# Performance work log

Hardware: AMD Instinct MI355X
Metric: run time of the kernel (lower is better)

## Reference

```python
import jax, jax.numpy as jnp
import numpy as np

B, N, D = 32, 256, 3
NF, L = 16, 3


def _fully_connected(n):
    # Same ordering as connect_fully: for i in range(n) for j in range(n) if i != j
    a = np.repeat(np.arange(n), n)
    b = np.tile(np.arange(n), n)
    m = a != b
    return a[m].astype(np.int32), b[m].astype(np.int32)


def setup_inputs() -> dict:
    key = jax.random.key(0)
    ks = jax.random.split(key, 12)
    src, dst = _fully_connected(N)
    s = 0.1  # small param scale for numerical stability
    return {
        "xs": jax.random.normal(ks[0], (B, N, D), jnp.float32),
        "vs": jax.random.normal(ks[1], (B, N, D), jnp.float32),
        "charges": jax.random.normal(ks[2], (B * N, 1), jnp.float32),
        "W_in": s * jax.random.normal(ks[3], (1, NF), jnp.float32),
        "b_in": jnp.zeros((NF,), jnp.float32),
        "W_v": s * jax.random.normal(ks[4], (L, NF, 1), jnp.float32),
        "We1": s * jax.random.normal(ks[5], (L, 2 * NF + 1, NF), jnp.float32),
        "be1": jnp.zeros((L, NF), jnp.float32),
        "We2": s * jax.random.normal(ks[6], (L, NF, NF), jnp.float32),
        "be2": jnp.zeros((L, NF), jnp.float32),
        "Wx": s * jax.random.normal(ks[7], (L, NF, 1), jnp.float32),
        "Wh1": s * jax.random.normal(ks[8], (L, 2 * NF, NF), jnp.float32),
        "bh1": jnp.zeros((L, NF), jnp.float32),
        "src": jnp.asarray(src),
        "dst": jnp.asarray(dst),
    }


def reference(xs, vs, charges, W_in, b_in, W_v, We1, be1, We2, be2, Wx, Wh1, bh1, src, dst):
    b, n, d = xs.shape
    # node scalar features from charges (ndata['f'])
    h = jax.nn.relu(charges.reshape(b, n, 1) @ W_in + b_in)  # [B,N,nf]
    x = xs
    n_layers = We1.shape[0]
    for l in range(n_layers):
        # fully-connected edge gather + subtract (edata['d'])
        de = x[:, dst] - x[:, src]                         # [B,E,3]
        r2 = jnp.sum(de * de, axis=-1, keepdims=True)      # [B,E,1]
        e_in = jnp.concatenate([h[:, src], h[:, dst], r2], axis=-1)  # [B,E,2nf+1]
        m = jax.nn.relu(e_in @ We1[l] + be1[l])
        m = jax.nn.relu(m @ We2[l] + be2[l])               # [B,E,nf]
        w = m @ Wx[l]                                      # [B,E,1]
        # equivariant coordinate update: scatter-add edge vectors into dst nodes
        agg_x = jnp.zeros_like(x).at[:, dst].add(de * w) / (n - 1)
        x = x + agg_x + vs * (h @ W_v[l])                  # velocity term (ndata['vel'])
        m_agg = jnp.zeros_like(h).at[:, dst].add(m)        # [B,N,nf]
        h = h + jax.nn.relu(jnp.concatenate([h, m_agg], axis=-1) @ Wh1[l] + bh1[l])
    # OurDynamics returns (se3_out['1'] + xs).view(-1, n_dimension)
    return x.reshape(-1, d)
```

## Files before the change

### kernel.cpp

```cpp
#include <hip/hip_runtime.h>

#define BB 32
#define NN 256
#define NF 16

typedef _Float16 half4 __attribute__((ext_vector_type(4)));
typedef float f32x4 __attribute__((ext_vector_type(4)));

#define X0_OFF 0
#define X1_OFF 32768
#define H0_OFF 65536
#define H1_OFF 196608
#define SU0_OFF 327680
#define SV0_OFF 458752
#define SU1_OFF 589824
#define SV1_OFF 720896
#define SU2_OFF 851968
#define SV2_OFF 983040

__global__ __launch_bounds__(256)
void init_kernel(const float* __restrict__ xs, const float* __restrict__ charges,
                 const float* __restrict__ W_in, const float* __restrict__ b_in,
                 const float* __restrict__ We1, const float* __restrict__ be1,
                 float* __restrict__ x0, float* __restrict__ h0,
                 float* __restrict__ su0, float* __restrict__ sv0) {
    __shared__ float sWs[256], sWd[256], sb1[NF];
    const int tid = threadIdx.x;
    sWs[tid] = We1[tid];
    sWd[tid] = We1[256 + tid];
    if (tid < NF) sb1[tid] = be1[tid];
    const int n = blockIdx.x * 256 + tid;
    const float c = charges[n];
    float h[NF];
#pragma unroll
    for (int f = 0; f < NF; ++f) {
        h[f] = fmaxf(fmaf(c, W_in[f], b_in[f]), 0.f);
        h0[n * NF + f] = h[f];
    }
    x0[n * 4 + 0] = xs[n * 3 + 0];
    x0[n * 4 + 1] = xs[n * 3 + 1];
    x0[n * 4 + 2] = xs[n * 3 + 2];
    x0[n * 4 + 3] = 0.f;
    __syncthreads();
#pragma unroll
    for (int k = 0; k < NF; ++k) {
        float u = 0.f, v = sb1[k];
#pragma unroll
        for (int f = 0; f < NF; ++f) {
            u = fmaf(h[f], sWs[f * NF + k], u);
            v = fmaf(h[f], sWd[f * NF + k], v);
        }
        su0[n * NF + k] = u;
        sv0[n * NF + k] = v;
    }
}

__global__ __launch_bounds__(256)
void layer_kernel(const float* __restrict__ x_in, const float* __restrict__ h_in,
                  const float* __restrict__ su_in, const float* __restrict__ sv_in,
                  float* __restrict__ x_out, float* __restrict__ h_out,
                  float* __restrict__ su_out, float* __restrict__ sv_out,
                  const float* __restrict__ vs, const float* __restrict__ Wv_l,
                  const float* __restrict__ We1_l, const float* __restrict__ We2_l,
                  const float* __restrict__ be2_l, const float* __restrict__ Wx_l,
                  const float* __restrict__ Wh1_l, const float* __restrict__ bh1_l,
                  const float* __restrict__ We1_n, const float* __restrict__ be1_n,
                  int final_layer) {
    __shared__ float sWh1s[512];
    __shared__ float sWa[256];
    __shared__ float sWb[256];
    __shared__ float sbe1n[NF];
    __shared__ float sh_new[8][NF + 1];
    __shared__ float sg[8][NF];

    const int tid  = threadIdx.x;
    const int b    = blockIdx.x >> 5;
    const int oct  = blockIdx.x & 31;
    const int n0l  = 8 * oct;
    const size_t n0 = (size_t)b * NN + n0l;
    const int w    = tid >> 6;
    const int lane = tid & 63;
    const int c    = lane & 15;
    const int g    = lane >> 4;

    sWh1s[tid]       = Wh1_l[tid];
    sWh1s[256 + tid] = Wh1_l[256 + tid];
    if (!final_layer) {
        const int f = tid >> 4, k = tid & 15;
        sWa[k * NF + f] = We1_n[tid];
        sWb[k * NF + f] = We1_n[256 + tid];
        if (tid < NF) sbe1n[tid] = be1_n[tid];
    }

    const int j0 = n0l + w, j1 = n0l + 4 + w;
    const float* x_b  = x_in + (size_t)b * NN * 4;
    const float* su_b = su_in + (size_t)b * NN * NF;
    const float4 xj0 = *(const float4*)(x_b + 4 * j0);
    const float4 xj1 = *(const float4*)(x_b + 4 * j1);
    half4 afrag;
    afrag.x = (_Float16)We2_l[(4 * g + 0) * NF + c];
    afrag.y = (_Float16)We2_l[(4 * g + 1) * NF + c];
    afrag.z = (_Float16)We2_l[(4 * g + 2) * NF + c];
    afrag.w = (_Float16)We2_l[(4 * g + 3) * NF + c];
    const float4 v40  = *(const float4*)(sv_in + ((size_t)b * NN + j0) * NF + 4 * g);
    const float4 v41  = *(const float4*)(sv_in + ((size_t)b * NN + j1) * NF + 4 * g);
    const float4 wr4  = *(const float4*)(We1_l + 512 + 4 * g);
    const float4 be2f = *(const float4*)(be2_l + 4 * g);
    const float4 wxf  = *(const float4*)(Wx_l + 4 * g);

    float Sw0 = 0.f, Swx0 = 0.f, Swy0 = 0.f, Swz0 = 0.f;
    float Sw1 = 0.f, Swx1 = 0.f, Swy1 = 0.f, Swz1 = 0.f;
    float g00 = 0.f, g01 = 0.f, g02 = 0.f, g03 = 0.f;
    float g10 = 0.f, g11 = 0.f, g12 = 0.f, g13 = 0.f;

    const float* su_p = su_b + c * NF + 4 * g;
    const float* x_p  = x_b + 4 * c;

#pragma unroll 2
    for (int t = 0; t < 16; ++t) {
        const float4 u4  = *(const float4*)(su_p + 256 * t);
        const float4 xs4 = *(const float4*)(x_p + 64 * t);
        const f32x4 zc = {0.f, 0.f, 0.f, 0.f};
        const int s = 16 * t + c;
        {
            const float dx = xj0.x - xs4.x, dy = xj0.y - xs4.y, dz = xj0.z - xs4.z;
            const float r2 = fmaf(dx, dx, fmaf(dy, dy, dz * dz));
            const float m0 = fmaxf(fmaf(r2, wr4.x, u4.x + v40.x), 0.f);
            const float m1 = fmaxf(fmaf(r2, wr4.y, u4.y + v40.y), 0.f);
            const float m2 = fmaxf(fmaf(r2, wr4.z, u4.z + v40.z), 0.f);
            const float m3 = fmaxf(fmaf(r2, wr4.w, u4.w + v40.w), 0.f);
            half4 bfrag;
            bfrag.x = (_Float16)m0; bfrag.y = (_Float16)m1;
            bfrag.z = (_Float16)m2; bfrag.w = (_Float16)m3;
            const f32x4 acc = __builtin_amdgcn_mfma_f32_16x16x16f16(afrag, bfrag, zc, 0, 0, 0);
            const float e0 = fmaxf(acc.x + be2f.x, 0.f);
            const float e1 = fmaxf(acc.y + be2f.y, 0.f);
            const float e2 = fmaxf(acc.z + be2f.z, 0.f);
            const float e3 = fmaxf(acc.w + be2f.w, 0.f);
            float wp = e0 * wxf.x;
            wp = fmaf(e1, wxf.y, wp);
            wp = fmaf(e2, wxf.z, wp);
            wp = fmaf(e3, wxf.w, wp);
            const float gsel = (s != j0) ? 1.f : 0.f;
            g00 = fmaf(e0, gsel, g00);
            g01 = fmaf(e1, gsel, g01);
            g02 = fmaf(e2, gsel, g02);
            g03 = fmaf(e3, gsel, g03);
            Sw0 += wp;
            Swx0 = fmaf(wp, xs4.x, Swx0);
            Swy0 = fmaf(wp, xs4.y, Swy0);
            Swz0 = fmaf(wp, xs4.z, Swz0);
        }
        {
            const float dx = xj1.x - xs4.x, dy = xj1.y - xs4.y, dz = xj1.z - xs4.z;
            const float r2 = fmaf(dx, dx, fmaf(dy, dy, dz * dz));
            const float m0 = fmaxf(fmaf(r2, wr4.x, u4.x + v41.x), 0.f);
            const float m1 = fmaxf(fmaf(r2, wr4.y, u4.y + v41.y), 0.f);
            const float m2 = fmaxf(fmaf(r2, wr4.z, u4.z + v41.z), 0.f);
            const float m3 = fmaxf(fmaf(r2, wr4.w, u4.w + v41.w), 0.f);
            half4 bfrag;
            bfrag.x = (_Float16)m0; bfrag.y = (_Float16)m1;
            bfrag.z = (_Float16)m2; bfrag.w = (_Float16)m3;
            const f32x4 acc = __builtin_amdgcn_mfma_f32_16x16x16f16(afrag, bfrag, zc, 0, 0, 0);
            const float e0 = fmaxf(acc.x + be2f.x, 0.f);
            const float e1 = fmaxf(acc.y + be2f.y, 0.f);
            const float e2 = fmaxf(acc.z + be2f.z, 0.f);
            const float e3 = fmaxf(acc.w + be2f.w, 0.f);
            float wp = e0 * wxf.x;
            wp = fmaf(e1, wxf.y, wp);
            wp = fmaf(e2, wxf.z, wp);
            wp = fmaf(e3, wxf.w, wp);
            const float gsel = (s != j1) ? 1.f : 0.f;
            g10 = fmaf(e0, gsel, g10);
            g11 = fmaf(e1, gsel, g11);
            g12 = fmaf(e2, gsel, g12);
            g13 = fmaf(e3, gsel, g13);
            Sw1 += wp;
            Swx1 = fmaf(wp, xs4.x, Swx1);
            Swy1 = fmaf(wp, xs4.y, Swy1);
            Swz1 = fmaf(wp, xs4.z, Swz1);
        }
    }

#pragma unroll
    for (int off = 1; off < 64; off <<= 1) {
        Sw0  += __shfl_xor(Sw0,  off, 64);  Sw1  += __shfl_xor(Sw1,  off, 64);
        Swx0 += __shfl_xor(Swx0, off, 64);  Swx1 += __shfl_xor(Swx1, off, 64);
        Swy0 += __shfl_xor(Swy0, off, 64);  Swy1 += __shfl_xor(Swy1, off, 64);
        Swz0 += __shfl_xor(Swz0, off, 64);  Swz1 += __shfl_xor(Swz1, off, 64);
    }
#pragma unroll
    for (int off = 1; off < 16; off <<= 1) {
        g00 += __shfl_xor(g00, off, 64);  g10 += __shfl_xor(g10, off, 64);
        g01 += __shfl_xor(g01, off, 64);  g11 += __shfl_xor(g11, off, 64);
        g02 += __shfl_xor(g02, off, 64);  g12 += __shfl_xor(g12, off, 64);
        g03 += __shfl_xor(g03, off, 64);  g13 += __shfl_xor(g13, off, 64);
    }
    if ((lane & 15) == 0) {
        *(float4*)&sg[w][4 * g]     = make_float4(g00, g01, g02, g03);
        *(float4*)&sg[w + 4][4 * g] = make_float4(g10, g11, g12, g13);
    }
    __syncthreads();

    const int is0 = (lane < 16);
    const int is1 = (lane >= 32 && lane < 48);
    if (is0 || is1) {
        const int f = lane & 15;
        const int slot = is0 ? w : (w + 4);
        const int jm   = is0 ? j0 : j1;
        const float SwS = is0 ? Sw0  : Sw1;
        const float SxS = is0 ? Swx0 : Swx1;
        const float SyS = is0 ? Swy0 : Swy1;
        const float SzS = is0 ? Swz0 : Swz1;
        const float4 xjm = is0 ? xj0 : xj1;
        const size_t nj = (size_t)b * NN + jm;
        float hd = bh1_l[f];
        float hv = 0.f;
#pragma unroll
        for (int k = 0; k < NF; ++k) {
            const float hjk = h_in[nj * NF + k];
            hd = fmaf(hjk, sWh1s[k * NF + f], hd);
            hv = fmaf(hjk, Wv_l[k], hv);
        }
#pragma unroll
        for (int k = 0; k < NF; ++k) {
            hd = fmaf(sg[slot][k], sWh1s[(NF + k) * NF + f], hd);
        }
        const float hnew = h_in[nj * NF + f] + fmaxf(hd, 0.f);
        sh_new[slot][f] = hnew;
        if (!final_layer) h_out[nj * NF + f] = hnew;
        if (f < 3) {
            const float xc = (f == 0) ? xjm.x : ((f == 1) ? xjm.y : xjm.z);
            const float Sc = (f == 0) ? SxS  : ((f == 1) ? SyS  : SzS);
            const float agg = (SwS * xc - Sc) * (1.f / 255.f);
            const float xnew = xc + agg + vs[nj * 3 + f] * hv;
            if (final_layer) x_out[nj * 3 + f] = xnew;
            else             x_out[nj * 4 + f] = xnew;
        }
        if (!final_layer && f == 3) x_out[nj * 4 + 3] = 0.f;
    }

    if (!final_layer) {
        __syncthreads();
        if (tid < 128) {
            const int jd = tid >> 4, k = tid & 15;
            float u = 0.f, v = sbe1n[k];
#pragma unroll
            for (int f = 0; f < NF; ++f) {
                const float hf = sh_new[jd][f];
                u = fmaf(hf, sWa[k * NF + f], u);
                v = fmaf(hf, sWb[k * NF + f], v);
            }
            su_out[(n0 + jd) * NF + k] = u;
            sv_out[(n0 + jd) * NF + k] = v;
        }
    }
}

extern "C" void kernel_launch(void* const* d_in, const int* in_sizes, int n_in,
                              void* d_out, int out_size, void* d_ws, size_t ws_size,
                              hipStream_t stream) {
    const float* xs      = (const float*)d_in[0];
    const float* vs      = (const float*)d_in[1];
    const float* charges = (const float*)d_in[2];
    const float* W_in    = (const float*)d_in[3];
    const float* b_in    = (const float*)d_in[4];
    const float* W_v     = (const float*)d_in[5];
    const float* We1     = (const float*)d_in[6];
    const float* be1     = (const float*)d_in[7];
    const float* We2     = (const float*)d_in[8];
    const float* be2     = (const float*)d_in[9];
    const float* Wx      = (const float*)d_in[10];
    const float* Wh1     = (const float*)d_in[11];
    const float* bh1     = (const float*)d_in[12];

    float* ws = (float*)d_ws;
    float* x0  = ws + X0_OFF;
    float* x1  = ws + X1_OFF;
    float* h0  = ws + H0_OFF;
    float* h1  = ws + H1_OFF;
    float* su0 = ws + SU0_OFF;
    float* sv0 = ws + SV0_OFF;
    float* su1 = ws + SU1_OFF;
    float* sv1 = ws + SV1_OFF;
    float* su2 = ws + SU2_OFF;
    float* sv2 = ws + SV2_OFF;
    float* out = (float*)d_out;

    hipLaunchKernelGGL(init_kernel, dim3(32), dim3(256), 0, stream,
                       xs, charges, W_in, b_in, We1, be1, x0, h0, su0, sv0);
    hipLaunchKernelGGL(layer_kernel, dim3(1024), dim3(256), 0, stream,
                       x0, h0, su0, sv0, x1, h1, su1, sv1,
                       vs, W_v + 0 * 16, We1 + 0 * 528, We2 + 0 * 256,
                       be2 + 0 * 16, Wx + 0 * 16, Wh1 + 0 * 512, bh1 + 0 * 16,
                       We1 + 1 * 528, be1 + 1 * 16, 0);
    hipLaunchKernelGGL(layer_kernel, dim3(1024), dim3(256), 0, stream,
                       x1, h1, su1, sv1, x0, h0, su2, sv2,
                       vs, W_v + 1 * 16, We1 + 1 * 528, We2 + 1 * 256,
                       be2 + 1 * 16, Wx + 1 * 16, Wh1 + 1 * 512, bh1 + 1 * 16,
                       We1 + 2 * 528, be1 + 2 * 16, 0);
    hipLaunchKernelGGL(layer_kernel, dim3(1024), dim3(256), 0, stream,
                       x0, h0, su2, sv2, out, h1, su1, sv1,
                       vs, W_v + 2 * 16, We1 + 2 * 528, We2 + 2 * 256,
                       be2 + 2 * 16, Wx + 2 * 16, Wh1 + 2 * 512, bh1 + 2 * 16,
                       We1 + 2 * 528, be1 + 2 * 16, 1);
}
```

Before: 135.7 us.

## Fuse init into first layer and recompute edge projections per block in LDS

```diff
diff --git a/kernel.cpp b/kernel.cpp
--- a/kernel.cpp
+++ b/kernel.cpp
@@ -11,67 +11,33 @@
 #define X1_OFF 32768
 #define H0_OFF 65536
 #define H1_OFF 196608
-#define SU0_OFF 327680
-#define SV0_OFF 458752
-#define SU1_OFF 589824
-#define SV1_OFF 720896
-#define SU2_OFF 851968
-#define SV2_OFF 983040
+
+__device__ __forceinline__ float dot4(float4 a, float4 b, float acc) {
+    acc = fmaf(a.x, b.x, acc); acc = fmaf(a.y, b.y, acc);
+    acc = fmaf(a.z, b.z, acc); acc = fmaf(a.w, b.w, acc);
+    return acc;
+}
 
 __global__ __launch_bounds__(256)
-void init_kernel(const float* __restrict__ xs, const float* __restrict__ charges,
-                 const float* __restrict__ W_in, const float* __restrict__ b_in,
-                 const float* __restrict__ We1, const float* __restrict__ be1,
-                 float* __restrict__ x0, float* __restrict__ h0,
-                 float* __restrict__ su0, float* __restrict__ sv0) {
-    __shared__ float sWs[256], sWd[256], sb1[NF];
-    const int tid = threadIdx.x;
-    sWs[tid] = We1[tid];
-    sWd[tid] = We1[256 + tid];
-    if (tid < NF) sb1[tid] = be1[tid];
-    const int n = blockIdx.x * 256 + tid;
-    const float c = charges[n];
-    float h[NF];
-#pragma unroll
-    for (int f = 0; f < NF; ++f) {
-        h[f] = fmaxf(fmaf(c, W_in[f], b_in[f]), 0.f);
-        h0[n * NF + f] = h[f];
-    }
-    x0[n * 4 + 0] = xs[n * 3 + 0];
-    x0[n * 4 + 1] = xs[n * 3 + 1];
-    x0[n * 4 + 2] = xs[n * 3 + 2];
-    x0[n * 4 + 3] = 0.f;
-    __syncthreads();
-#pragma unroll
-    for (int k = 0; k < NF; ++k) {
-        float u = 0.f, v = sb1[k];
-#pragma unroll
-        for (int f = 0; f < NF; ++f) {
-            u = fmaf(h[f], sWs[f * NF + k], u);
-            v = fmaf(h[f], sWd[f * NF + k], v);
-        }
-        su0[n * NF + k] = u;
-        sv0[n * NF + k] = v;
-    }
-}
-
-__global__ __launch_bounds__(256)
-void layer_kernel(const float* __restrict__ x_in, const float* __restrict__ h_in,
-                  const float* __restrict__ su_in, const float* __restrict__ sv_in,
+void layer_kernel(const float* __restrict__ xs, const float* __restrict__ charges,
+                  const float* __restrict__ W_in, const float* __restrict__ b_in,
+                  const float* __restrict__ x_in, const float* __restrict__ h_in,
                   float* __restrict__ x_out, float* __restrict__ h_out,
-                  float* __restrict__ su_out, float* __restrict__ sv_out,
                   const float* __restrict__ vs, const float* __restrict__ Wv_l,
-                  const float* __restrict__ We1_l, const float* __restrict__ We2_l,
-                  const float* __restrict__ be2_l, const float* __restrict__ Wx_l,
-                  const float* __restrict__ Wh1_l, const float* __restrict__ bh1_l,
-                  const float* __restrict__ We1_n, const float* __restrict__ be1_n,
-                  int final_layer) {
-    __shared__ float sWh1s[512];
-    __shared__ float sWa[256];
-    __shared__ float sWb[256];
-    __shared__ float sbe1n[NF];
-    __shared__ float sh_new[8][NF + 1];
-    __shared__ float sg[8][NF];
+                  const float* __restrict__ We1_l, const float* __restrict__ be1_l,
+                  const float* __restrict__ We2_l, const float* __restrict__ be2_l,
+                  const float* __restrict__ Wx_l, const float* __restrict__ Wh1_l,
+                  const float* __restrict__ bh1_l,
+                  int first_layer, int final_layer) {
+    __shared__ __align__(16) float  su[NN * 20];
+    __shared__ __align__(16) float4 sx[NN];
+    __shared__ __align__(16) float  sWaT[256];
+    __shared__ __align__(16) float  sWbT[256];
+    __shared__ float  sWh1s[512];
+    __shared__ __align__(16) float  sh8[8][NF];
+    __shared__ float  svd[8][NF];
+    __shared__ float  sg[8][NF];
+    __shared__ float  sWin[NF], sbin[NF], sbe1[NF];
 
     const int tid  = threadIdx.x;
     const int b    = blockIdx.x >> 5;
@@ -83,45 +49,118 @@
     const int c    = lane & 15;
     const int g    = lane >> 4;
 
+    {
+        const int f = tid >> 4, k = tid & 15;
+        sWaT[k * NF + f] = We1_l[tid];
+        sWbT[k * NF + f] = We1_l[256 + tid];
+    }
     sWh1s[tid]       = Wh1_l[tid];
     sWh1s[256 + tid] = Wh1_l[256 + tid];
-    if (!final_layer) {
-        const int f = tid >> 4, k = tid & 15;
-        sWa[k * NF + f] = We1_n[tid];
-        sWb[k * NF + f] = We1_n[256 + tid];
-        if (tid < NF) sbe1n[tid] = be1_n[tid];
-    }
-
-    const int j0 = n0l + w, j1 = n0l + 4 + w;
-    const float* x_b  = x_in + (size_t)b * NN * 4;
-    const float* su_b = su_in + (size_t)b * NN * NF;
-    const float4 xj0 = *(const float4*)(x_b + 4 * j0);
-    const float4 xj1 = *(const float4*)(x_b + 4 * j1);
+    if (tid < NF) {
+        sbe1[tid] = be1_l[tid];
+        if (first_layer) { sWin[tid] = W_in[tid]; sbin[tid] = b_in[tid]; }
+    }
+    if (first_layer) {
+        const size_t n = (size_t)b * NN + tid;
+        sx[tid] = make_float4(xs[n * 3 + 0], xs[n * 3 + 1], xs[n * 3 + 2], 0.f);
+        if (tid < 128) {
+            const int jd = tid >> 4, f = tid & 15;
+            sh8[jd][f] = fmaxf(fmaf(charges[n0 + jd], W_in[f], b_in[f]), 0.f);
+        }
+    } else {
+        sx[tid] = ((const float4*)x_in)[(size_t)b * NN + tid];
+        if (tid < 32) {
+            const int jd = tid >> 2, q = tid & 3;
+            *(float4*)&sh8[jd][4 * q] =
+                ((const float4*)(h_in + (n0 + jd) * NF))[q];
+        }
+    }
+    __syncthreads();
+
+    {
+        float4 hq0, hq1, hq2, hq3;
+        if (first_layer) {
+            const float cc = charges[(size_t)b * NN + tid];
+            hq0 = make_float4(fmaxf(fmaf(cc, sWin[0], sbin[0]), 0.f),
+                              fmaxf(fmaf(cc, sWin[1], sbin[1]), 0.f),
+                              fmaxf(fmaf(cc, sWin[2], sbin[2]), 0.f),
+                              fmaxf(fmaf(cc, sWin[3], sbin[3]), 0.f));
+            hq1 = make_float4(fmaxf(fmaf(cc, sWin[4], sbin[4]), 0.f),
+                              fmaxf(fmaf(cc, sWin[5], sbin[5]), 0.f),
+                              fmaxf(fmaf(cc, sWin[6], sbin[6]), 0.f),
+                              fmaxf(fmaf(cc, sWin[7], sbin[7]), 0.f));
+            hq2 = make_float4(fmaxf(fmaf(cc, sWin[8], sbin[8]), 0.f),
+                              fmaxf(fmaf(cc, sWin[9], sbin[9]), 0.f),
+                              fmaxf(fmaf(cc, sWin[10], sbin[10]), 0.f),
+                              fmaxf(fmaf(cc, sWin[11], sbin[11]), 0.f));
+            hq3 = make_float4(fmaxf(fmaf(cc, sWin[12], sbin[12]), 0.f),
+                              fmaxf(fmaf(cc, sWin[13], sbin[13]), 0.f),
+                              fmaxf(fmaf(cc, sWin[14], sbin[14]), 0.f),
+                              fmaxf(fmaf(cc, sWin[15], sbin[15]), 0.f));
+        } else {
+            const float4* h4 = (const float4*)(h_in + ((size_t)b * NN + tid) * NF);
+            hq0 = h4[0]; hq1 = h4[1]; hq2 = h4[2]; hq3 = h4[3];
+        }
+#pragma unroll
+        for (int q = 0; q < 4; ++q) {
+            float4 uq;
+            {
+                const float4* wt = (const float4*)&sWaT[(4 * q + 0) * NF];
+                uq.x = dot4(hq3, wt[3], dot4(hq2, wt[2], dot4(hq1, wt[1], dot4(hq0, wt[0], 0.f))));
+            }
+            {
+                const float4* wt = (const float4*)&sWaT[(4 * q + 1) * NF];
+                uq.y = dot4(hq3, wt[3], dot4(hq2, wt[2], dot4(hq1, wt[1], dot4(hq0, wt[0], 0.f))));
+            }
+            {
+                const float4* wt = (const float4*)&sWaT[(4 * q + 2) * NF];
+                uq.z = dot4(hq3, wt[3], dot4(hq2, wt[2], dot4(hq1, wt[1], dot4(hq0, wt[0], 0.f))));
+            }
+            {
+                const float4* wt = (const float4*)&sWaT[(4 * q + 3) * NF];
+                uq.w = dot4(hq3, wt[3], dot4(hq2, wt[2], dot4(hq1, wt[1], dot4(hq0, wt[0], 0.f))));
+            }
+            *(float4*)&su[tid * 20 + 4 * q] = uq;
+        }
+    }
+    if (tid < 128) {
+        const int jd = tid >> 4, k = tid & 15;
+        const float4* hj = (const float4*)&sh8[jd][0];
+        const float4* wt = (const float4*)&sWbT[k * NF];
+        float v = sbe1[k];
+        v = dot4(hj[0], wt[0], v);
+        v = dot4(hj[1], wt[1], v);
+        v = dot4(hj[2], wt[2], v);
+        v = dot4(hj[3], wt[3], v);
+        svd[jd][k] = v;
+    }
     half4 afrag;
     afrag.x = (_Float16)We2_l[(4 * g + 0) * NF + c];
     afrag.y = (_Float16)We2_l[(4 * g + 1) * NF + c];
     afrag.z = (_Float16)We2_l[(4 * g + 2) * NF + c];
     afrag.w = (_Float16)We2_l[(4 * g + 3) * NF + c];
-    const float4 v40  = *(const float4*)(sv_in + ((size_t)b * NN + j0) * NF + 4 * g);
-    const float4 v41  = *(const float4*)(sv_in + ((size_t)b * NN + j1) * NF + 4 * g);
     const float4 wr4  = *(const float4*)(We1_l + 512 + 4 * g);
     const float4 be2f = *(const float4*)(be2_l + 4 * g);
     const float4 wxf  = *(const float4*)(Wx_l + 4 * g);
+    __syncthreads();
+
+    const int j0 = n0l + w, j1 = n0l + 4 + w;
+    const float4 xj0 = sx[j0];
+    const float4 xj1 = sx[j1];
+    const float4 v40 = *(const float4*)&svd[w][4 * g];
+    const float4 v41 = *(const float4*)&svd[w + 4][4 * g];
 
     float Sw0 = 0.f, Swx0 = 0.f, Swy0 = 0.f, Swz0 = 0.f;
     float Sw1 = 0.f, Swx1 = 0.f, Swy1 = 0.f, Swz1 = 0.f;
     float g00 = 0.f, g01 = 0.f, g02 = 0.f, g03 = 0.f;
     float g10 = 0.f, g11 = 0.f, g12 = 0.f, g13 = 0.f;
 
-    const float* su_p = su_b + c * NF + 4 * g;
-    const float* x_p  = x_b + 4 * c;
-
 #pragma unroll 2
     for (int t = 0; t < 16; ++t) {
-        const float4 u4  = *(const float4*)(su_p + 256 * t);
-        const float4 xs4 = *(const float4*)(x_p + 64 * t);
+        const int s = 16 * t + c;
+        const float4 u4  = *(const float4*)&su[s * 20 + 4 * g];
+        const float4 xs4 = sx[s];
         const f32x4 zc = {0.f, 0.f, 0.f, 0.f};
-        const int s = 16 * t + c;
         {
             const float dx = xj0.x - xs4.x, dy = xj0.y - xs4.y, dz = xj0.z - xs4.z;
             const float r2 = fmaf(dx, dx, fmaf(dy, dy, dz * dz));
@@ -218,7 +257,7 @@
         float hv = 0.f;
 #pragma unroll
         for (int k = 0; k < NF; ++k) {
-            const float hjk = h_in[nj * NF + k];
+            const float hjk = sh8[slot][k];
             hd = fmaf(hjk, sWh1s[k * NF + f], hd);
             hv = fmaf(hjk, Wv_l[k], hv);
         }
@@ -226,8 +265,7 @@
         for (int k = 0; k < NF; ++k) {
             hd = fmaf(sg[slot][k], sWh1s[(NF + k) * NF + f], hd);
         }
-        const float hnew = h_in[nj * NF + f] + fmaxf(hd, 0.f);
-        sh_new[slot][f] = hnew;
+        const float hnew = sh8[slot][f] + fmaxf(hd, 0.f);
         if (!final_layer) h_out[nj * NF + f] = hnew;
         if (f < 3) {
             const float xc = (f == 0) ? xjm.x : ((f == 1) ? xjm.y : xjm.z);
@@ -238,22 +276,6 @@
             else             x_out[nj * 4 + f] = xnew;
         }
         if (!final_layer && f == 3) x_out[nj * 4 + 3] = 0.f;
-    }
-
-    if (!final_layer) {
-        __syncthreads();
-        if (tid < 128) {
-            const int jd = tid >> 4, k = tid & 15;
-            float u = 0.f, v = sbe1n[k];
-#pragma unroll
-            for (int f = 0; f < NF; ++f) {
-                const float hf = sh_new[jd][f];
-                u = fmaf(hf, sWa[k * NF + f], u);
-                v = fmaf(hf, sWb[k * NF + f], v);
-            }
-            su_out[(n0 + jd) * NF + k] = u;
-            sv_out[(n0 + jd) * NF + k] = v;
-        }
     }
 }
 
@@ -275,33 +297,22 @@
     const float* bh1     = (const float*)d_in[12];
 
     float* ws = (float*)d_ws;
-    float* x0  = ws + X0_OFF;
-    float* x1  = ws + X1_OFF;
-    float* h0  = ws + H0_OFF;
-    float* h1  = ws + H1_OFF;
-    float* su0 = ws + SU0_OFF;
-    float* sv0 = ws + SV0_OFF;
-    float* su1 = ws + SU1_OFF;
-    float* sv1 = ws + SV1_OFF;
-    float* su2 = ws + SU2_OFF;
-    float* sv2 = ws + SV2_OFF;
+    float* x0 = ws + X0_OFF;
+    float* x1 = ws + X1_OFF;
+    float* h0 = ws + H0_OFF;
+    float* h1 = ws + H1_OFF;
     float* out = (float*)d_out;
 
-    hipLaunchKernelGGL(init_kernel, dim3(32), dim3(256), 0, stream,
-                       xs, charges, W_in, b_in, We1, be1, x0, h0, su0, sv0);
     hipLaunchKernelGGL(layer_kernel, dim3(1024), dim3(256), 0, stream,
-                       x0, h0, su0, sv0, x1, h1, su1, sv1,
-                       vs, W_v + 0 * 16, We1 + 0 * 528, We2 + 0 * 256,
-                       be2 + 0 * 16, Wx + 0 * 16, Wh1 + 0 * 512, bh1 + 0 * 16,
-                       We1 + 1 * 528, be1 + 1 * 16, 0);
+                       xs, charges, W_in, b_in, x0, h0, x1, h1,
+                       vs, W_v + 0 * 16, We1 + 0 * 528, be1 + 0 * 16, We2 + 0 * 256,
+                       be2 + 0 * 16, Wx + 0 * 16, Wh1 + 0 * 512, bh1 + 0 * 16, 1, 0);
     hipLaunchKernelGGL(layer_kernel, dim3(1024), dim3(256), 0, stream,
-                       x1, h1, su1, sv1, x0, h0, su2, sv2,
-                       vs, W_v + 1 * 16, We1 + 1 * 528, We2 + 1 * 256,
-                       be2 + 1 * 16, Wx + 1 * 16, Wh1 + 1 * 512, bh1 + 1 * 16,
-                       We1 + 2 * 528, be1 + 2 * 16, 0);
+                       xs, charges, W_in, b_in, x1, h1, x0, h0,
+                       vs, W_v + 1 * 16, We1 + 1 * 528, be1 + 1 * 16, We2 + 1 * 256,
+                       be2 + 1 * 16, Wx + 1 * 16, Wh1 + 1 * 512, bh1 + 1 * 16, 0, 0);
     hipLaunchKernelGGL(layer_kernel, dim3(1024), dim3(256), 0, stream,
-                       x0, h0, su2, sv2, out, h1, su1, sv1,
-                       vs, W_v + 2 * 16, We1 + 2 * 528, We2 + 2 * 256,
-                       be2 + 2 * 16, Wx + 2 * 16, Wh1 + 2 * 512, bh1 + 2 * 16,
-                       We1 + 2 * 528, be1 + 2 * 16, 1);
+                       xs, charges, W_in, b_in, x0, h0, out, h1,
+                       vs, W_v + 2 * 16, We1 + 2 * 528, be1 + 2 * 16, We2 + 2 * 256,
+                       be2 + 2 * 16, Wx + 2 * 16, Wh1 + 2 * 512, bh1 + 2 * 16, 0, 1);
 }
```

Result: slower. 143.0 us (+5.3%).
